# Kernel tuning notes

Measured on AMD Instinct MI355X. Metric: run time of the kernel, lower is better.

Reference implementation:

```python
import jax, jax.numpy as jnp
import numpy as np

N, D, V = 16384, 2048, 8192  # rows, code bits, val_range (codebook size)


def setup_inputs() -> dict:
    key = jax.random.key(0)
    k1, k2 = jax.random.split(key)
    x = jax.random.normal(k1, (N, D), dtype=jnp.float32)   # encoded rows
    di = jax.random.normal(k2, (D, V), dtype=jnp.float32)  # decode codebook (fwd.di)
    return {"x": x, "di": di}


def reference(x, di):
    # Original loops over rows doing (1,D)@(D,V) then argmax; batched this is one
    # GEMM [N,D]@[D,V] -> [N,V] followed by argmax over the V axis, cast to float32
    # (the torch code stores the index into a float32 output tensor).
    scores = jnp.matmul(x, di)                  # [N, V]
    return jnp.argmax(scores, axis=1).astype(jnp.float32)  # [N]
```

## Files before the change

### kernel.cpp

```cpp
#include <hip/hip_runtime.h>

typedef _Float16 f16x8 __attribute__((ext_vector_type(8)));
typedef float f32x4 __attribute__((ext_vector_type(4)));
typedef float f32x16 __attribute__((ext_vector_type(16)));
typedef int i32x4 __attribute__((ext_vector_type(4)));
typedef int i32x8 __attribute__((ext_vector_type(8)));

__device__ __forceinline__ unsigned int fkey(float f) {
    unsigned int u = __float_as_uint(f);
    return u ^ ((u & 0x80000000u) ? 0xFFFFFFFFu : 0x80000000u);
}
__device__ __forceinline__ float unkey(unsigned int k) {
    unsigned int u = (k & 0x80000000u) ? (k ^ 0x80000000u) : ~k;
    return __uint_as_float(u);
}

__device__ __forceinline__ unsigned int f32_to_e4m3(float f) {
    float a = fabsf(f);
    a = fminf(a, 448.0f);
    unsigned int s = (__float_as_uint(f) >> 24) & 0x80u;
    if (a < 0.015625f) {
        int m = (int)rintf(a * 512.0f);
        return s | (unsigned int)m;
    }
    int e = ilogbf(a);
    float step = ldexpf(1.0f, e - 3);
    int q = (int)rintf(a / step);
    if (q == 16) { e += 1; q = 8; }
    return s | (unsigned int)(((e + 7) << 3) | (q - 8));
}

__global__ __launch_bounds__(256) void prep_x_q(
    const float* __restrict__ x, unsigned char* __restrict__ Xq)
{
    size_t base = ((size_t)blockIdx.x * 256 + threadIdx.x) * 8;
    float4 a0 = *(const float4*)(x + base);
    float4 a1 = *(const float4*)(x + base + 4);
    float v[8] = {a0.x, a0.y, a0.z, a0.w, a1.x, a1.y, a1.z, a1.w};
    unsigned long long b = 0;
#pragma unroll
    for (int j = 0; j < 8; ++j)
        b |= (unsigned long long)f32_to_e4m3(v[j]) << (8 * j);
    *(unsigned long long*)(Xq + base) = b;
}

__global__ __launch_bounds__(256) void prep_di_q(
    const float* __restrict__ di, unsigned char* __restrict__ DqT,
    _Float16* __restrict__ DhT, _Float16* __restrict__ DlT, int D, int V)
{
    int v  = blockIdx.x * 64 + (threadIdx.x & 63);
    int d0 = blockIdx.y * 32 + (threadIdx.x >> 6) * 8;
    f16x8 h, l;
    unsigned long long b = 0;
#pragma unroll
    for (int j = 0; j < 8; ++j) {
        float val = di[(size_t)(d0 + j) * V + v];
        _Float16 hh = (_Float16)val;
        h[j] = hh;
        l[j] = (_Float16)(val - (float)hh);
        b |= (unsigned long long)f32_to_e4m3(val) << (8 * j);
    }
    *(unsigned long long*)(DqT + (size_t)v * D + d0) = b;
    *(f16x8*)(DhT + (size_t)v * D + d0) = h;
    *(f16x8*)(DlT + (size_t)v * D + d0) = l;
}

__global__ __launch_bounds__(256, 4) void gemm_mx_top2(
    const unsigned char* __restrict__ Xq, const unsigned char* __restrict__ DqT,
    unsigned long long* __restrict__ cand, int N, int D, int V)
{
    __shared__ __align__(16) unsigned char sm[32768];

    const int tid = threadIdx.x;
    const int w = tid >> 6, lane = tid & 63;
    const int wr = w >> 1, wc = w & 1;
    const int l31 = lane & 31, hl = lane >> 5;

    const int xcd = blockIdx.x & 7;
    const int s   = blockIdx.x >> 3;
    const int sl  = xcd * 16 + (s >> 6);
    const int in  = s & 63;
    const int bm  = ((sl >> 3) * 8 + (in >> 3)) * 128;
    const int bn  = ((sl & 7) * 8 + (in & 7)) * 128;

    const int srow_in = lane >> 2;
    const int sp      = lane & 3;

    const unsigned char* srcbase[4];
    int dstoff[4];
#pragma unroll
    for (int i = 0; i < 4; ++i) {
        const int c = w * 4 + i;
        const int isB = (c >= 8);
        const int cc = isB ? c - 8 : c;
        const int row = cc * 16 + srow_in;
        const int slog = sp ^ ((row >> 1) & 3);
        srcbase[i] = (isB ? DqT + (size_t)(bn + row) * D
                          : Xq + (size_t)(bm + row) * D) + slog * 16;
        dstoff[i] = (isB ? 8192 : 0) + cc * 1024;
    }

    auto stage = [&](int buf, int k0) {
#pragma unroll
        for (int i = 0; i < 4; ++i) {
            __builtin_amdgcn_global_load_lds(
                (const __attribute__((address_space(1))) void*)(srcbase[i] + k0),
                (__attribute__((address_space(3))) void*)
                    (sm + buf * 16384 + dstoff[i]),
                16, 0, 0);
        }
    };
    auto ldfrag = [&](int buf, int op, int r) -> i32x8 {
        const unsigned char* base =
            sm + buf * 16384 + (op ? 8192 : 0) + (r >> 4) * 1024 + (r & 15) * 64;
        const int sw = (r >> 1) & 3;
        i32x4 lo = *(const i32x4*)(base + (((hl << 1)    ) ^ sw) * 16);
        i32x4 hi = *(const i32x4*)(base + (((hl << 1) | 1) ^ sw) * 16);
        return __builtin_shufflevector(lo, hi, 0, 1, 2, 3, 4, 5, 6, 7);
    };

    f32x16 acc[2][2];
#pragma unroll
    for (int fm = 0; fm < 2; ++fm)
#pragma unroll
        for (int fn = 0; fn < 2; ++fn)
#pragma unroll
            for (int q = 0; q < 16; ++q) acc[fm][fn][q] = 0.0f;

    const int nt = D / 64;
    int cb = 0;

    stage(0, 0);
    __syncthreads();

#pragma unroll 1
    for (int t = 0; t < nt; ++t) {
        if (t + 1 < nt) stage(cb ^ 1, (t + 1) * 64);

        i32x8 b0 = ldfrag(cb, 1, wc * 64 + l31);
        i32x8 b1 = ldfrag(cb, 1, wc * 64 + 32 + l31);
        i32x8 a0 = ldfrag(cb, 0, wr * 64 + l31);
        i32x8 a1 = ldfrag(cb, 0, wr * 64 + 32 + l31);
        acc[0][0] = __builtin_amdgcn_mfma_scale_f32_32x32x64_f8f6f4(
            a0, b0, acc[0][0], 0, 0, 0, 0x7F7F7F7F, 0, 0x7F7F7F7F);
        acc[0][1] = __builtin_amdgcn_mfma_scale_f32_32x32x64_f8f6f4(
            a0, b1, acc[0][1], 0, 0, 0, 0x7F7F7F7F, 0, 0x7F7F7F7F);
        acc[1][0] = __builtin_amdgcn_mfma_scale_f32_32x32x64_f8f6f4(
            a1, b0, acc[1][0], 0, 0, 0, 0x7F7F7F7F, 0, 0x7F7F7F7F);
        acc[1][1] = __builtin_amdgcn_mfma_scale_f32_32x32x64_f8f6f4(
            a1, b1, acc[1][1], 0, 0, 0, 0x7F7F7F7F, 0, 0x7F7F7F7F);

        __syncthreads();
        cb ^= 1;
    }

#pragma unroll
    for (int fm = 0; fm < 2; ++fm)
#pragma unroll
        for (int j = 0; j < 16; ++j) {
            const int row = bm + wr * 64 + fm * 32 + (j & 3) + 8 * (j >> 2) + 4 * hl;
            const int c0 = bn + wc * 64 + l31;
            unsigned long long p0 =
                ((unsigned long long)fkey(acc[fm][0][j]) << 32) |
                (unsigned long long)(0xFFFFFFFFu - (unsigned int)c0);
            unsigned long long p1 =
                ((unsigned long long)fkey(acc[fm][1][j]) << 32) |
                (unsigned long long)(0xFFFFFFFFu - (unsigned int)(c0 + 32));
            unsigned long long t1 = p0 > p1 ? p0 : p1;
            unsigned long long t2 = p0 > p1 ? p1 : p0;
#pragma unroll
            for (int m = 1; m < 32; m <<= 1) {
                unsigned long long o1 = __shfl_xor(t1, m);
                unsigned long long o2 = __shfl_xor(t2, m);
                unsigned long long n1 = t1 > o1 ? t1 : o1;
                unsigned long long lo = t1 > o1 ? o1 : t1;
                unsigned long long m2 = t2 > o2 ? t2 : o2;
                t2 = lo > m2 ? lo : m2;
                t1 = n1;
            }
            if (l31 == 0) {
                size_t ci = ((size_t)row * 128 + (bn >> 6) + wc) * 2;
                cand[ci] = t1;
                cand[ci + 1] = t2;
            }
        }
}

#define DELTA 10.0f

__global__ __launch_bounds__(256) void refine_kernel(
    const unsigned long long* __restrict__ cand,
    const float* __restrict__ X,
    const _Float16* __restrict__ DhT, const _Float16* __restrict__ DlT,
    float* __restrict__ out, int N, int D, int V)
{
    const int w = threadIdx.x >> 6, lane = threadIdx.x & 63;
    const int r = blockIdx.x * 4 + w;
    if (r >= N) return;

    const int nent = 256;
    const unsigned long long* cr = cand + (size_t)r * nent;

    unsigned long long p[4];
#pragma unroll
    for (int i = 0; i < 4; ++i) p[i] = cr[lane * 4 + i];

    unsigned long long pmax = p[0];
#pragma unroll
    for (int i = 1; i < 4; ++i) if (p[i] > pmax) pmax = p[i];
#pragma unroll
    for (int m = 1; m < 64; m <<= 1) {
        unsigned long long o = __shfl_xor(pmax, m);
        if (o > pmax) pmax = o;
    }

    const float s1 = unkey((unsigned int)(pmax >> 32));
    const unsigned int kthr = fkey(s1 - DELTA);

    int cnt = 0;
    unsigned long long masks[4];
#pragma unroll
    for (int i = 0; i < 4; ++i) {
        masks[i] = __ballot((unsigned int)(p[i] >> 32) >= kthr);
        cnt += __popcll(masks[i]);
    }

    if (cnt <= 1) {
        if (lane == 0)
            out[r] = (float)(0xFFFFFFFFu - (unsigned int)(pmax & 0xFFFFFFFFull));
        return;
    }

    const float* xrow = X + (size_t)r * D;
    float xbuf[32];
#pragma unroll
    for (int q = 0; q < 8; ++q) {
        float4 xv = *(const float4*)(xrow + lane * 32 + q * 4);
        xbuf[q * 4 + 0] = xv.x; xbuf[q * 4 + 1] = xv.y;
        xbuf[q * 4 + 2] = xv.z; xbuf[q * 4 + 3] = xv.w;
    }

    unsigned long long bestp = 0;
    for (int i = 0; i < 4; ++i) {
        unsigned long long mask = masks[i];
        while (mask) {
            const int src = __ffsll((unsigned long long)mask) - 1;
            mask &= mask - 1;
            const unsigned long long cp = __shfl(p[i], src);
            const int col = (int)(0xFFFFFFFFu - (unsigned int)(cp & 0xFFFFFFFFull));

            const f16x8* dh = (const f16x8*)(DhT + (size_t)col * D) + lane * 4;
            const f16x8* dl = (const f16x8*)(DlT + (size_t)col * D) + lane * 4;
            float s = 0.0f;
#pragma unroll
            for (int q = 0; q < 4; ++q) {
                f16x8 h = dh[q], l = dl[q];
#pragma unroll
                for (int e = 0; e < 8; ++e)
                    s = fmaf(xbuf[q * 8 + e], (float)h[e] + (float)l[e], s);
            }
#pragma unroll
            for (int m = 1; m < 64; m <<= 1) s += __shfl_xor(s, m);

            const unsigned long long pp =
                ((unsigned long long)fkey(s) << 32) |
                (unsigned long long)(0xFFFFFFFFu - (unsigned int)col);
            if (pp > bestp) bestp = pp;
        }
    }
    if (lane == 0)
        out[r] = (float)(0xFFFFFFFFu - (unsigned int)(bestp & 0xFFFFFFFFull));
}

#define FBK 16
#define FTM 8
#define FTN 8

__global__ __launch_bounds__(256) void gemm_argmax_fp32_kernel(
    const float* __restrict__ A, const float* __restrict__ B,
    unsigned long long* __restrict__ best, int N, int D, int V)
{
    __shared__ float As[FBK][128 + 4];
    __shared__ float Bs[FBK][128 + 4];

    const int tid = threadIdx.x;
    const int tx = tid & 15;
    const int ty = tid >> 4;
    const int bm = blockIdx.y * 128;
    const int bn = blockIdx.x * 128;

    const int arow  = tid >> 2;
    const int acol4 = tid & 3;
    const int brow  = tid >> 5;
    const int bcol4 = tid & 31;

    float acc[FTM][FTN];
#pragma unroll
    for (int i = 0; i < FTM; ++i)
#pragma unroll
        for (int j = 0; j < FTN; ++j) acc[i][j] = 0.0f;

    for (int k0 = 0; k0 < D; k0 += FBK) {
        float4 a0 = *reinterpret_cast<const float4*>(&A[(size_t)(bm + arow) * D + k0 + acol4 * 4]);
        float4 a1 = *reinterpret_cast<const float4*>(&A[(size_t)(bm + arow + 64) * D + k0 + acol4 * 4]);
        float4 b0 = *reinterpret_cast<const float4*>(&B[(size_t)(k0 + brow) * V + bn + bcol4 * 4]);
        float4 b1 = *reinterpret_cast<const float4*>(&B[(size_t)(k0 + brow + 8) * V + bn + bcol4 * 4]);

        As[acol4 * 4 + 0][arow] = a0.x;
        As[acol4 * 4 + 1][arow] = a0.y;
        As[acol4 * 4 + 2][arow] = a0.z;
        As[acol4 * 4 + 3][arow] = a0.w;
        As[acol4 * 4 + 0][arow + 64] = a1.x;
        As[acol4 * 4 + 1][arow + 64] = a1.y;
        As[acol4 * 4 + 2][arow + 64] = a1.z;
        As[acol4 * 4 + 3][arow + 64] = a1.w;
        *reinterpret_cast<float4*>(&Bs[brow][bcol4 * 4]) = b0;
        *reinterpret_cast<float4*>(&Bs[brow + 8][bcol4 * 4]) = b1;

        __syncthreads();
#pragma unroll
        for (int kk = 0; kk < FBK; ++kk) {
            float4 av0 = *reinterpret_cast<const float4*>(&As[kk][ty * FTM]);
            float4 av1 = *reinterpret_cast<const float4*>(&As[kk][ty * FTM + 4]);
            float4 bv0 = *reinterpret_cast<const float4*>(&Bs[kk][tx * FTN]);
            float4 bv1 = *reinterpret_cast<const float4*>(&Bs[kk][tx * FTN + 4]);
            float a[FTM] = {av0.x, av0.y, av0.z, av0.w, av1.x, av1.y, av1.z, av1.w};
            float b[FTN] = {bv0.x, bv0.y, bv0.z, bv0.w, bv1.x, bv1.y, bv1.z, bv1.w};
#pragma unroll
            for (int i = 0; i < FTM; ++i)
#pragma unroll
                for (int j = 0; j < FTN; ++j)
                    acc[i][j] = fmaf(a[i], b[j], acc[i][j]);
        }
        __syncthreads();
    }

#pragma unroll
    for (int i = 0; i < FTM; ++i) {
        float bv = acc[i][0];
        int bc = bn + tx * FTN;
#pragma unroll
        for (int j = 1; j < FTN; ++j) {
            float v = acc[i][j];
            int c = bn + tx * FTN + j;
            if (v > bv) { bv = v; bc = c; }
        }
        unsigned long long packed =
            ((unsigned long long)fkey(bv) << 32) |
            (unsigned long long)(0xFFFFFFFFu - (unsigned int)bc);
#pragma unroll
        for (int m = 1; m < 16; m <<= 1) {
            unsigned long long o = __shfl_xor(packed, m, 16);
            if (o > packed) packed = o;
        }
        if (tx == 0) atomicMax(&best[bm + ty * FTM + i], packed);
    }
}

__global__ void decode_kernel(const unsigned long long* __restrict__ best,
                              float* __restrict__ out, int N)
{
    int i = blockIdx.x * blockDim.x + threadIdx.x;
    if (i < N) {
        unsigned int inv = (unsigned int)(best[i] & 0xFFFFFFFFull);
        out[i] = (float)(0xFFFFFFFFu - inv);
    }
}

extern "C" void kernel_launch(void* const* d_in, const int* in_sizes, int n_in,
                              void* d_out, int out_size, void* d_ws, size_t ws_size,
                              hipStream_t stream) {
    const float* A = (const float*)d_in[0];
    const float* B = (const float*)d_in[1];
    float* out = (float*)d_out;

    const int N = out_size;
    const int D = in_sizes[0] / N;
    const int V = in_sizes[1] / D;

    const size_t szXq = (size_t)N * D;
    const size_t szDq = (size_t)D * V;
    const size_t szDh = (size_t)D * V * sizeof(_Float16);
    const size_t candsz = (size_t)N * 256 * 8;
    const size_t need = szXq + szDq + 2 * szDh + candsz;

    if (ws_size >= need) {
        char* wsp = (char*)d_ws;
        unsigned char* Xq  = (unsigned char*)(wsp);
        unsigned char* DqT = (unsigned char*)(wsp + szXq);
        _Float16* DhT = (_Float16*)(wsp + szXq + szDq);
        _Float16* DlT = (_Float16*)(wsp + szXq + szDq + szDh);
        unsigned long long* cand =
            (unsigned long long*)(wsp + szXq + szDq + 2 * szDh);

        prep_x_q<<<(int)(((size_t)N * D) / (256 * 8)), 256, 0, stream>>>(A, Xq);
        prep_di_q<<<dim3(V / 64, D / 32), 256, 0, stream>>>(B, DqT, DhT, DlT, D, V);
        gemm_mx_top2<<<(N / 128) * (V / 128), 256, 0, stream>>>(
            Xq, DqT, cand, N, D, V);
        refine_kernel<<<(N + 3) / 4, 256, 0, stream>>>(
            cand, A, DhT, DlT, out, N, D, V);
    } else {
        unsigned long long* best = (unsigned long long*)d_ws;
        hipMemsetAsync(best, 0, (size_t)N * sizeof(unsigned long long), stream);
        gemm_argmax_fp32_kernel<<<dim3(V / 128, N / 128), 256, 0, stream>>>(A, B, best, N, D, V);
        decode_kernel<<<(N + 255) / 256, 256, 0, stream>>>(best, out, N);
    }
}
```

Baseline: 617.2 us.

## Give each wave private LDS tiles and replace block barriers with waitcnt pipelining

The fp8 GEMM stops sharing A/B tiles across the four waves of a block. Each wave now stages its own 64-row A and B slices into a private 16KB LDS region, and loads are ordered with s_waitcnt vmcnt/lgkmcnt instead of __syncthreads. The loads are prefetched two k-steps ahead. This removes block-wide barrier stalls, at the cost of doubling global/L2 load traffic per block and doubling LDS use, which cuts the occupancy hint from 4 to 2 blocks.

New measurement: 763.2 us. 23.6% more time.

```diff
diff --git a/kernel.cpp b/kernel.cpp
--- a/kernel.cpp
+++ b/kernel.cpp
@@ -65,15 +65,14 @@
     *(f16x8*)(DlT + (size_t)v * D + d0) = l;
 }
 
-__global__ __launch_bounds__(256, 4) void gemm_mx_top2(
+__global__ __launch_bounds__(256, 2) void gemm_mx_top2(
     const unsigned char* __restrict__ Xq, const unsigned char* __restrict__ DqT,
     unsigned long long* __restrict__ cand, int N, int D, int V)
 {
-    __shared__ __align__(16) unsigned char sm[32768];
+    __shared__ __align__(16) unsigned char sm[65536];
 
     const int tid = threadIdx.x;
     const int w = tid >> 6, lane = tid & 63;
-    const int wr = w >> 1, wc = w & 1;
     const int l31 = lane & 31, hl = lane >> 5;
 
     const int xcd = blockIdx.x & 7;
@@ -83,36 +82,39 @@
     const int bm  = ((sl >> 3) * 8 + (in >> 3)) * 128;
     const int bn  = ((sl & 7) * 8 + (in & 7)) * 128;
 
+    const int wrow = bm + (w >> 1) * 64;
+    const int wcol = bn + (w & 1) * 64;
+    unsigned char* wlds = sm + w * 16384;
+
     const int srow_in = lane >> 2;
     const int sp      = lane & 3;
 
-    const unsigned char* srcbase[4];
-    int dstoff[4];
-#pragma unroll
-    for (int i = 0; i < 4; ++i) {
-        const int c = w * 4 + i;
-        const int isB = (c >= 8);
-        const int cc = isB ? c - 8 : c;
+    const unsigned char* srcbase[8];
+    int dstoff[8];
+#pragma unroll
+    for (int i = 0; i < 8; ++i) {
+        const int op = i >> 2;
+        const int cc = i & 3;
         const int row = cc * 16 + srow_in;
         const int slog = sp ^ ((row >> 1) & 3);
-        srcbase[i] = (isB ? DqT + (size_t)(bn + row) * D
-                          : Xq + (size_t)(bm + row) * D) + slog * 16;
-        dstoff[i] = (isB ? 8192 : 0) + cc * 1024;
+        srcbase[i] = (op ? DqT + (size_t)(wcol + row) * D
+                         : Xq + (size_t)(wrow + row) * D) + slog * 16;
+        dstoff[i] = op * 4096 + cc * 1024;
     }
 
     auto stage = [&](int buf, int k0) {
 #pragma unroll
-        for (int i = 0; i < 4; ++i) {
+        for (int i = 0; i < 8; ++i) {
             __builtin_amdgcn_global_load_lds(
                 (const __attribute__((address_space(1))) void*)(srcbase[i] + k0),
                 (__attribute__((address_space(3))) void*)
-                    (sm + buf * 16384 + dstoff[i]),
+                    (wlds + buf * 8192 + dstoff[i]),
                 16, 0, 0);
         }
     };
     auto ldfrag = [&](int buf, int op, int r) -> i32x8 {
         const unsigned char* base =
-            sm + buf * 16384 + (op ? 8192 : 0) + (r >> 4) * 1024 + (r & 15) * 64;
+            wlds + buf * 8192 + op * 4096 + (r >> 4) * 1024 + (r & 15) * 64;
         const int sw = (r >> 1) & 3;
         i32x4 lo = *(const i32x4*)(base + (((hl << 1)    ) ^ sw) * 16);
         i32x4 hi = *(const i32x4*)(base + (((hl << 1) | 1) ^ sw) * 16);
@@ -131,16 +133,20 @@
     int cb = 0;
 
     stage(0, 0);
-    __syncthreads();
+    stage(1, 64);
 
 #pragma unroll 1
     for (int t = 0; t < nt; ++t) {
-        if (t + 1 < nt) stage(cb ^ 1, (t + 1) * 64);
-
-        i32x8 b0 = ldfrag(cb, 1, wc * 64 + l31);
-        i32x8 b1 = ldfrag(cb, 1, wc * 64 + 32 + l31);
-        i32x8 a0 = ldfrag(cb, 0, wr * 64 + l31);
-        i32x8 a1 = ldfrag(cb, 0, wr * 64 + 32 + l31);
+        if (t + 1 < nt) {
+            asm volatile("s_waitcnt vmcnt(8)" ::: "memory");
+        } else {
+            asm volatile("s_waitcnt vmcnt(0)" ::: "memory");
+        }
+
+        i32x8 b0 = ldfrag(cb, 1, l31);
+        i32x8 b1 = ldfrag(cb, 1, 32 + l31);
+        i32x8 a0 = ldfrag(cb, 0, l31);
+        i32x8 a1 = ldfrag(cb, 0, 32 + l31);
         acc[0][0] = __builtin_amdgcn_mfma_scale_f32_32x32x64_f8f6f4(
             a0, b0, acc[0][0], 0, 0, 0, 0x7F7F7F7F, 0, 0x7F7F7F7F);
         acc[0][1] = __builtin_amdgcn_mfma_scale_f32_32x32x64_f8f6f4(
@@ -150,7 +156,8 @@
         acc[1][1] = __builtin_amdgcn_mfma_scale_f32_32x32x64_f8f6f4(
             a1, b1, acc[1][1], 0, 0, 0, 0x7F7F7F7F, 0, 0x7F7F7F7F);
 
-        __syncthreads();
+        asm volatile("s_waitcnt lgkmcnt(0)" ::: "memory");
+        if (t + 2 < nt) stage(cb, (t + 2) * 64);
         cb ^= 1;
     }
 
@@ -158,8 +165,8 @@
     for (int fm = 0; fm < 2; ++fm)
 #pragma unroll
         for (int j = 0; j < 16; ++j) {
-            const int row = bm + wr * 64 + fm * 32 + (j & 3) + 8 * (j >> 2) + 4 * hl;
-            const int c0 = bn + wc * 64 + l31;
+            const int row = wrow + fm * 32 + (j & 3) + 8 * (j >> 2) + 4 * hl;
+            const int c0 = wcol + l31;
             unsigned long long p0 =
                 ((unsigned long long)fkey(acc[fm][0][j]) << 32) |
                 (unsigned long long)(0xFFFFFFFFu - (unsigned int)c0);
@@ -179,7 +186,7 @@
                 t1 = n1;
             }
             if (l31 == 0) {
-                size_t ci = ((size_t)row * 128 + (bn >> 6) + wc) * 2;
+                size_t ci = ((size_t)row * 128 + (wcol >> 6)) * 2;
                 cand[ci] = t1;
                 cand[ci + 1] = t2;
             }
```
